# Performance work log

Measured on AMD Instinct MI355X. Metric: run time of the kernel, lower is better.

## Reference

```python
import jax, jax.numpy as jnp
import numpy as np

NUM_HEADS = 16


def setup_inputs() -> dict:
    key = jax.random.key(0)
    ks = jax.random.split(key, 7)
    T, B, E = 2048, 2, 1024
    return {
        "query": jax.random.normal(ks[0], (T, B, E), jnp.float32),
        "key": jax.random.normal(ks[1], (T, B, E), jnp.float32),
        "value": jax.random.normal(ks[2], (T, B, E), jnp.float32),
        "query_pos": jax.random.normal(ks[3], (T, B, E), jnp.float32),
        "key_pos": jax.random.normal(ks[4], (T, B, E), jnp.float32),
        "W": jax.random.normal(ks[5], (E, E), jnp.float32) * (1.0 / np.sqrt(E)),
        "b": jax.random.normal(ks[6], (E,), jnp.float32) * 0.01,
    }


def reference(query, key, value, query_pos, key_pos, W, b):
    T, B, E = query.shape
    S = key.shape[0]
    H = NUM_HEADS
    D = E // H
    scale = jnp.asarray(D ** 0.5, query.dtype)

    identity = query  # residual uses query BEFORE positional add
    q = query + query_pos
    k = key + key_pos

    # (T,B,E) -> (B,H,T,D)
    q = q.reshape(T, B, H, D).transpose(1, 2, 0, 3)
    k = k.reshape(S, B, H, D).transpose(1, 2, 0, 3)
    v = value.reshape(S, B, H, D).transpose(1, 2, 0, 3)

    attn = jnp.einsum("bhtd,bhsd->bhts", q, k) / scale
    attn = jax.nn.softmax(attn, axis=-1)  # dropout p=0 -> identity

    out = jnp.einsum("bhts,bhsd->bhtd", attn, v)
    out = out.transpose(2, 0, 1, 3).reshape(T, B, E)  # (B,H,T,D)->(T,B,E)
    out = out @ W.T + b  # fuse_heads linear; out_dropout p=0 -> identity
    out = out + identity

    attn_avg = attn.sum(axis=1) / H  # average over heads -> (B,T,S)
    return out, attn_avg
```

## Files before the change

### kernel.cpp

```cpp
#include <hip/hip_runtime.h>
#include <hip/hip_bf16.h>

#define T_DIM 2048
#define S_DIM 2048
#define B_DIM 2
#define E_DIM 1024
#define H_DIM 16
#define D_DIM 64
#define EXP2S 0.18033688f
#define EXP2(x) __builtin_amdgcn_exp2f(x)

typedef unsigned short u16;
typedef unsigned int u32;
typedef float v4f __attribute__((ext_vector_type(4)));
typedef short v8s __attribute__((ext_vector_type(8)));
typedef short v4s __attribute__((ext_vector_type(4)));

__device__ __forceinline__ u16 f2bf(float f) {
    union { float f; u32 u; } x; x.f = f;
    return (u16)((x.u + 0x7fffu + ((x.u >> 16) & 1u)) >> 16);
}
__device__ __forceinline__ u32 pkrn(float lo, float hi) {
    union { __hip_bfloat162 h; u32 u; } c;
    c.h = __float22bfloat162_rn(make_float2(lo, hi));
    return c.u;
}
__device__ __forceinline__ v4f mfma16(v8s a, v8s b, v4f c) {
    return __builtin_amdgcn_mfma_f32_16x16x32_bf16(a, b, c, 0, 0, 0);
}
__device__ __forceinline__ v4f mfma16x16(v4s a, v4s b, v4f c) {
    return __builtin_amdgcn_mfma_f32_16x16x16bf16_1k(a, b, c, 0, 0, 0);
}
__device__ __forceinline__ v8s ld8(const u16* p) {
    return *reinterpret_cast<const v8s*>(p);
}

__global__ __launch_bounds__(256) void prep_qk(
    const float* __restrict__ q, const float* __restrict__ qp,
    const float* __restrict__ k, const float* __restrict__ kp,
    const float* __restrict__ W,
    u16* __restrict__ qb, u16* __restrict__ ks, u16* __restrict__ Wb) {
    int o = blockIdx.x * 256 + threadIdx.x;
    int d = o & 63, t = (o >> 6) & 2047, h = (o >> 17) & 15, b = o >> 21;
    int src = ((t * B_DIM + b) << 10) + (h << 6) + d;
    qb[o] = f2bf((q[src] + qp[src]) * EXP2S);
    ks[o] = f2bf(k[src] + kp[src]);
    if (o < E_DIM * E_DIM) Wb[o] = f2bf(W[o]);
}

__global__ __launch_bounds__(256) void prep_vt(const float* __restrict__ V, u16* __restrict__ vt) {
    __shared__ float tile[64 * 65];
    int bx = blockIdx.x;
    int bh = bx >> 5;
    int s0 = (bx & 31) * 64;
    int b = bh >> 4, h = bh & 15;
    int tid = threadIdx.x;
    int quarter = tid >> 6, c = tid & 63;
    int boff = b * E_DIM + h * 64;
#pragma unroll
    for (int p = 0; p < 16; ++p) {
        int r = quarter * 16 + p;
        tile[r * 65 + c] = V[(size_t)(s0 + r) * (B_DIM * E_DIM) + boff + c];
    }
    __syncthreads();
#pragma unroll
    for (int p = 0; p < 16; ++p) {
        int d = quarter * 16 + p;
        vt[(size_t)bh * (D_DIM * S_DIM) + (size_t)d * S_DIM + s0 + c] = f2bf(tile[c * 65 + d]);
    }
}

#define PITCH 72
__global__ __launch_bounds__(256) void attn_pv(
    const u16* __restrict__ qb, const u16* __restrict__ ks, const u16* __restrict__ vt,
    float* __restrict__ lin, u16* __restrict__ Xb) {
    __shared__ u16 Kl[2][64 * PITCH];
    __shared__ u16 Vl[2][64 * PITCH];

    int bx = blockIdx.x;
    int bh = bx >> 4;
    int b = bh >> 4, h = bh & 15;
    int tid = threadIdx.x;
    int w = tid >> 6;
    int tbase = (bx & 15) * 128 + w * 32;
    int lane = tid & 63;
    int m = lane & 15, g = lane >> 4;

    int srow = tid >> 2;
    int sqtr = (tid & 3) * 16;

    uint4 kr0, kr1, vr0, vr1;
    auto load_stage = [&](int s0) {
        const uint4* kp = reinterpret_cast<const uint4*>(
            ks + ((size_t)bh * S_DIM + s0 + srow) * 64 + sqtr);
        kr0 = kp[0]; kr1 = kp[1];
        const uint4* vp = reinterpret_cast<const uint4*>(
            vt + (size_t)bh * (D_DIM * S_DIM) + (size_t)srow * S_DIM + s0 + sqtr);
        vr0 = vp[0]; vr1 = vp[1];
    };
    auto write_stage = [&](int buf) {
        uint4* kd = reinterpret_cast<uint4*>(&Kl[buf][srow * PITCH + sqtr]);
        kd[0] = kr0; kd[1] = kr1;
        uint4* vd = reinterpret_cast<uint4*>(&Vl[buf][srow * PITCH + sqtr]);
        vd[0] = vr0; vd[1] = vr1;
    };

    const u16* qrow = qb + ((size_t)bh * T_DIM + tbase + m) * 64 + g * 8;
    v8s aq[2][2];
    aq[0][0] = ld8(qrow);        aq[0][1] = ld8(qrow + 32);
    aq[1][0] = ld8(qrow + 1024); aq[1][1] = ld8(qrow + 1024 + 32);

    v4f O[2][4];
    float lacc[2] = {0.f, 0.f};
#pragma unroll
    for (int tr = 0; tr < 2; ++tr)
#pragma unroll
        for (int dd = 0; dd < 4; ++dd) O[tr][dd] = (v4f){0.f, 0.f, 0.f, 0.f};

    load_stage(0);
    write_stage(0);
    load_stage(64);
    __syncthreads();

    for (int it = 0; it < 32; ++it) {
        int buf = it & 1;
        const u16* Kb = Kl[buf];
        const u16* Vb = Vl[buf];
#pragma unroll
        for (int ss = 0; ss < 4; ++ss) {
            v8s kf0 = ld8(&Kb[(ss * 16 + m) * PITCH + g * 8]);
            v8s kf1 = ld8(&Kb[(ss * 16 + m) * PITCH + 32 + g * 8]);
            v4s pa0, pa1;
            {
                v4f z = {0.f, 0.f, 0.f, 0.f};
                z = mfma16(kf0, aq[0][0], z);
                z = mfma16(kf1, aq[0][1], z);
                float e0 = EXP2(z[0]);
                float e1 = EXP2(z[1]);
                float e2 = EXP2(z[2]);
                float e3 = EXP2(z[3]);
                lacc[0] += (e0 + e1) + (e2 + e3);
                union { u32 u[2]; v4s s; } pk_;
                pk_.u[0] = pkrn(e0, e1);
                pk_.u[1] = pkrn(e2, e3);
                pa0 = pk_.s;
            }
            {
                v4f z = {0.f, 0.f, 0.f, 0.f};
                z = mfma16(kf0, aq[1][0], z);
                z = mfma16(kf1, aq[1][1], z);
                float e0 = EXP2(z[0]);
                float e1 = EXP2(z[1]);
                float e2 = EXP2(z[2]);
                float e3 = EXP2(z[3]);
                lacc[1] += (e0 + e1) + (e2 + e3);
                union { u32 u[2]; v4s s; } pk_;
                pk_.u[0] = pkrn(e0, e1);
                pk_.u[1] = pkrn(e2, e3);
                pa1 = pk_.s;
            }
            __builtin_amdgcn_s_setprio(1);
#pragma unroll
            for (int dd = 0; dd < 4; ++dd) {
                v4s bv = *reinterpret_cast<const v4s*>(
                    &Vb[(dd * 16 + m) * PITCH + ss * 16 + g * 4]);
                O[0][dd] = mfma16x16(pa0, bv, O[0][dd]);
                O[1][dd] = mfma16x16(pa1, bv, O[1][dd]);
            }
            __builtin_amdgcn_s_setprio(0);
        }
        if (it + 1 < 32) {
            write_stage(buf ^ 1);
            if (it + 2 < 32) load_stage((it + 2) * 64);
        }
        __syncthreads();
    }

#pragma unroll
    for (int tr = 0; tr < 2; ++tr) {
        lacc[tr] += __shfl_xor(lacc[tr], 16);
        lacc[tr] += __shfl_xor(lacc[tr], 32);
        float linv = 1.0f / lacc[tr];
        if (lane < 16) lin[(size_t)bh * T_DIM + tbase + tr * 16 + m] = linv;
#pragma unroll
        for (int r = 0; r < 4; ++r) {
            float lr = __shfl(linv, g * 4 + r);
            int t = tbase + tr * 16 + g * 4 + r;
#pragma unroll
            for (int dd = 0; dd < 4; ++dd)
                Xb[((size_t)t * B_DIM + b) * E_DIM + h * 64 + dd * 16 + m] =
                    f2bf(O[tr][dd][r] * lr);
        }
    }
}

__global__ __launch_bounds__(256, 4) void attn_avg(
    const u16* __restrict__ qb, const u16* __restrict__ ks,
    const float* __restrict__ lin, float* __restrict__ out1) {
    __shared__ u16 Kl[2][64 * PITCH];
    int bx = blockIdx.x;
    int b = bx >> 9;
    int tt = (bx >> 5) & 15;
    int st = bx & 31;
    int tid = threadIdx.x;
    int w = tid >> 6;
    int tbase = tt * 128 + w * 32;
    int sbase = st * 64;
    int lane = tid & 63, m = lane & 15, g = lane >> 4;

    int srow = tid >> 2;
    int sqtr = (tid & 3) * 16;

    uint4 kr0, kr1;
    auto load_stage = [&](int h) {
        const uint4* kp = reinterpret_cast<const uint4*>(
            ks + ((size_t)(b * 16 + h) * S_DIM + sbase + srow) * 64 + sqtr);
        kr0 = kp[0]; kr1 = kp[1];
    };
    auto write_stage = [&](int buf) {
        uint4* kd = reinterpret_cast<uint4*>(&Kl[buf][srow * PITCH + sqtr]);
        kd[0] = kr0; kd[1] = kr1;
    };

    v8s aqc00, aqc01, aqc10, aqc11, aqn00, aqn01, aqn10, aqn11;
    float livc[2][4], livn[2][4];
    auto load_q = [&](int h, v8s& a00, v8s& a01, v8s& a10, v8s& a11, float (&liv)[2][4]) {
        int bh = b * 16 + h;
        const u16* qrow = qb + ((size_t)bh * T_DIM + tbase + m) * 64 + g * 8;
        a00 = ld8(qrow);        a01 = ld8(qrow + 32);
        a10 = ld8(qrow + 1024); a11 = ld8(qrow + 1024 + 32);
#pragma unroll
        for (int tr = 0; tr < 2; ++tr)
#pragma unroll
            for (int r = 0; r < 4; ++r)
                liv[tr][r] = lin[(size_t)bh * T_DIM + tbase + tr * 16 + g * 4 + r] * (1.0f / 16.0f);
    };

    v4f AVG[2][4];
#pragma unroll
    for (int tr = 0; tr < 2; ++tr)
#pragma unroll
        for (int ss = 0; ss < 4; ++ss) AVG[tr][ss] = (v4f){0.f, 0.f, 0.f, 0.f};

    load_stage(0);
    write_stage(0);
    load_stage(1);
    load_q(0, aqc00, aqc01, aqc10, aqc11, livc);
    __syncthreads();

    for (int h = 0; h < H_DIM; ++h) {
        int buf = h & 1;
        if (h + 1 < H_DIM) load_q(h + 1, aqn00, aqn01, aqn10, aqn11, livn);

        const u16* Kb = Kl[buf];
#pragma unroll
        for (int ss = 0; ss < 4; ++ss) {
            v8s kf0 = ld8(&Kb[(ss * 16 + m) * PITCH + g * 8]);
            v8s kf1 = ld8(&Kb[(ss * 16 + m) * PITCH + 32 + g * 8]);
            {
                v4f z = {0.f, 0.f, 0.f, 0.f};
                z = mfma16(aqc00, kf0, z);
                z = mfma16(aqc01, kf1, z);
#pragma unroll
                for (int r = 0; r < 4; ++r)
                    AVG[0][ss][r] += EXP2(z[r]) * livc[0][r];
            }
            {
                v4f z = {0.f, 0.f, 0.f, 0.f};
                z = mfma16(aqc10, kf0, z);
                z = mfma16(aqc11, kf1, z);
#pragma unroll
                for (int r = 0; r < 4; ++r)
                    AVG[1][ss][r] += EXP2(z[r]) * livc[1][r];
            }
        }
        if (h + 1 < H_DIM) {
            write_stage(buf ^ 1);
            if (h + 2 < H_DIM) load_stage(h + 2);
        }
        __syncthreads();
        aqc00 = aqn00; aqc01 = aqn01; aqc10 = aqn10; aqc11 = aqn11;
#pragma unroll
        for (int tr = 0; tr < 2; ++tr)
#pragma unroll
            for (int r = 0; r < 4; ++r) livc[tr][r] = livn[tr][r];
    }
#pragma unroll
    for (int tr = 0; tr < 2; ++tr)
#pragma unroll
        for (int ss = 0; ss < 4; ++ss)
#pragma unroll
            for (int r = 0; r < 4; ++r) {
                int t = tbase + tr * 16 + g * 4 + r;
                out1[((size_t)b * T_DIM + t) * S_DIM + sbase + ss * 16 + m] = AVG[tr][ss][r];
            }
}

__global__ __launch_bounds__(256) void linear_mfma(
    const u16* __restrict__ Xb, const u16* __restrict__ Wb,
    const float* __restrict__ bias, const float* __restrict__ query,
    float* __restrict__ out0) {
    __shared__ u16 Al[2][64 * PITCH];
    __shared__ u16 Wl[2][128 * PITCH];
    int bx = blockIdx.x;
    int it = bx >> 3, jt = bx & 7;
    int tid = threadIdx.x;
    int w = tid >> 6;
    int lane = tid & 63;
    int m = lane & 15, g = lane >> 4;

    int arow = tid >> 2, aq4 = (tid & 3) * 16;
    int wrow = tid >> 1, wh2 = (tid & 1) * 32;

    uint4 ar0, ar1, wr0, wr1, wr2, wr3;
    auto load_stage = [&](int k0) {
        const uint4* ap = reinterpret_cast<const uint4*>(
            Xb + (size_t)(it * 64 + arow) * E_DIM + k0 + aq4);
        ar0 = ap[0]; ar1 = ap[1];
        const uint4* wp = reinterpret_cast<const uint4*>(
            Wb + (size_t)(jt * 128 + wrow) * E_DIM + k0 + wh2);
        wr0 = wp[0]; wr1 = wp[1]; wr2 = wp[2]; wr3 = wp[3];
    };
    auto write_stage = [&](int buf) {
        uint4* ad = reinterpret_cast<uint4*>(&Al[buf][arow * PITCH + aq4]);
        ad[0] = ar0; ad[1] = ar1;
        uint4* wd = reinterpret_cast<uint4*>(&Wl[buf][wrow * PITCH + wh2]);
        wd[0] = wr0; wd[1] = wr1; wd[2] = wr2; wd[3] = wr3;
    };

    v4f acc[4][2];
#pragma unroll
    for (int tr = 0; tr < 4; ++tr)
#pragma unroll
        for (int nn = 0; nn < 2; ++nn) acc[tr][nn] = (v4f){0.f, 0.f, 0.f, 0.f};

    load_stage(0);
    write_stage(0);
    load_stage(64);
    __syncthreads();

    for (int itk = 0; itk < 16; ++itk) {
        int buf = itk & 1;
        const u16* Ab = Al[buf];
        const u16* Ws = Wl[buf];
        v8s af[4][2], wf[2][2];
#pragma unroll
        for (int tr = 0; tr < 4; ++tr) {
            af[tr][0] = ld8(&Ab[(tr * 16 + m) * PITCH + g * 8]);
            af[tr][1] = ld8(&Ab[(tr * 16 + m) * PITCH + 32 + g * 8]);
        }
#pragma unroll
        for (int nn = 0; nn < 2; ++nn) {
            wf[nn][0] = ld8(&Ws[((w * 2 + nn) * 16 + m) * PITCH + g * 8]);
            wf[nn][1] = ld8(&Ws[((w * 2 + nn) * 16 + m) * PITCH + 32 + g * 8]);
        }
#pragma unroll
        for (int tr = 0; tr < 4; ++tr)
#pragma unroll
            for (int nn = 0; nn < 2; ++nn) {
                acc[tr][nn] = mfma16(af[tr][0], wf[nn][0], acc[tr][nn]);
                acc[tr][nn] = mfma16(af[tr][1], wf[nn][1], acc[tr][nn]);
            }
        if (itk + 1 < 16) {
            write_stage(buf ^ 1);
            if (itk + 2 < 16) load_stage((itk + 2) * 64);
        }
        __syncthreads();
    }

#pragma unroll
    for (int tr = 0; tr < 4; ++tr)
#pragma unroll
        for (int nn = 0; nn < 2; ++nn) {
            int col = jt * 128 + (w * 2 + nn) * 16 + m;
            float bv = bias[col];
#pragma unroll
            for (int r = 0; r < 4; ++r) {
                int row = it * 64 + tr * 16 + g * 4 + r;
                out0[(size_t)row * E_DIM + col] =
                    acc[tr][nn][r] + bv + query[(size_t)row * E_DIM + col];
            }
        }
}

extern "C" void kernel_launch(void* const* d_in, const int* in_sizes, int n_in,
                              void* d_out, int out_size, void* d_ws, size_t ws_size,
                              hipStream_t stream) {
    const float* query = (const float*)d_in[0];
    const float* key   = (const float*)d_in[1];
    const float* value = (const float*)d_in[2];
    const float* qpos  = (const float*)d_in[3];
    const float* kpos  = (const float*)d_in[4];
    const float* W     = (const float*)d_in[5];
    const float* bias  = (const float*)d_in[6];

    char* ws = (char*)d_ws;
    u16*   qb  = (u16*)(ws);
    u16*   ks  = (u16*)(ws + (size_t)( 8u << 20));
    u16*   vt  = (u16*)(ws + (size_t)(16u << 20));
    u16*   Wb  = (u16*)(ws + (size_t)(24u << 20));
    float* lin = (float*)(ws + (size_t)(26u << 20));
    u16*   Xb  = (u16*)(ws + (size_t)(27u << 20));

    float* out0 = (float*)d_out;
    float* out1 = out0 + (size_t)T_DIM * B_DIM * E_DIM;

    prep_qk<<<(B_DIM * H_DIM * T_DIM * D_DIM) / 256, 256, 0, stream>>>(query, qpos, key, kpos, W, qb, ks, Wb);
    prep_vt<<<B_DIM * H_DIM * (S_DIM / 64), 256, 0, stream>>>(value, vt);
    attn_pv<<<B_DIM * H_DIM * (T_DIM / 128), 256, 0, stream>>>(qb, ks, vt, lin, Xb);
    attn_avg<<<B_DIM * (T_DIM / 128) * (S_DIM / 64), 256, 0, stream>>>(qb, ks, lin, out1);
    linear_mfma<<<(T_DIM * B_DIM / 64) * (E_DIM / 128), 256, 0, stream>>>(Xb, Wb, bias, query, out0);
}
```

Baseline: 258.8 us.

## Merge prep kernels and co-schedule attention-average with output linear in one launch

Combines the Q/K/W conversion and V transpose into a single launch with a block-index split. Likewise merges the head-averaged attention kernel with the output projection GEMM so their blocks can run concurrently, since neither depends on the other. The linear part now uses a 32-wide K step with a smaller LDS pitch so it fits the shared-memory budget of the avg part. It also drops the s_setprio hints in attn_pv. This trades launch overhead and tail idle time for more loop iterations and barriers in the GEMM.

```diff
diff --git a/kernel.cpp b/kernel.cpp
--- a/kernel.cpp
+++ b/kernel.cpp
@@ -35,26 +35,28 @@
     return *reinterpret_cast<const v8s*>(p);
 }
 
-__global__ __launch_bounds__(256) void prep_qk(
+__global__ __launch_bounds__(256) void prep_all(
     const float* __restrict__ q, const float* __restrict__ qp,
     const float* __restrict__ k, const float* __restrict__ kp,
-    const float* __restrict__ W,
-    u16* __restrict__ qb, u16* __restrict__ ks, u16* __restrict__ Wb) {
-    int o = blockIdx.x * 256 + threadIdx.x;
-    int d = o & 63, t = (o >> 6) & 2047, h = (o >> 17) & 15, b = o >> 21;
-    int src = ((t * B_DIM + b) << 10) + (h << 6) + d;
-    qb[o] = f2bf((q[src] + qp[src]) * EXP2S);
-    ks[o] = f2bf(k[src] + kp[src]);
-    if (o < E_DIM * E_DIM) Wb[o] = f2bf(W[o]);
-}
-
-__global__ __launch_bounds__(256) void prep_vt(const float* __restrict__ V, u16* __restrict__ vt) {
+    const float* __restrict__ W, const float* __restrict__ V,
+    u16* __restrict__ qb, u16* __restrict__ ks, u16* __restrict__ Wb,
+    u16* __restrict__ vt) {
     __shared__ float tile[64 * 65];
     int bx = blockIdx.x;
-    int bh = bx >> 5;
-    int s0 = (bx & 31) * 64;
+    int tid = threadIdx.x;
+    if (bx < 16384) {
+        int o = bx * 256 + tid;
+        int d = o & 63, t = (o >> 6) & 2047, h = (o >> 17) & 15, b = o >> 21;
+        int src = ((t * B_DIM + b) << 10) + (h << 6) + d;
+        qb[o] = f2bf((q[src] + qp[src]) * EXP2S);
+        ks[o] = f2bf(k[src] + kp[src]);
+        if (o < E_DIM * E_DIM) Wb[o] = f2bf(W[o]);
+        return;
+    }
+    int vb = bx - 16384;
+    int bh = vb >> 5;
+    int s0 = (vb & 31) * 64;
     int b = bh >> 4, h = bh & 15;
-    int tid = threadIdx.x;
     int quarter = tid >> 6, c = tid & 63;
     int boff = b * E_DIM + h * 64;
 #pragma unroll
@@ -159,7 +161,6 @@
                 pk_.u[1] = pkrn(e2, e3);
                 pa1 = pk_.s;
             }
-            __builtin_amdgcn_s_setprio(1);
 #pragma unroll
             for (int dd = 0; dd < 4; ++dd) {
                 v4s bv = *reinterpret_cast<const v4s*>(
@@ -167,7 +168,6 @@
                 O[0][dd] = mfma16x16(pa0, bv, O[0][dd]);
                 O[1][dd] = mfma16x16(pa1, bv, O[1][dd]);
             }
-            __builtin_amdgcn_s_setprio(0);
         }
         if (it + 1 < 32) {
             write_stage(buf ^ 1);
@@ -194,138 +194,136 @@
     }
 }
 
-__global__ __launch_bounds__(256, 4) void attn_avg(
+#define PITCHL 40
+__global__ __launch_bounds__(256, 4) void avg_linear(
     const u16* __restrict__ qb, const u16* __restrict__ ks,
-    const float* __restrict__ lin, float* __restrict__ out1) {
-    __shared__ u16 Kl[2][64 * PITCH];
-    int bx = blockIdx.x;
-    int b = bx >> 9;
-    int tt = (bx >> 5) & 15;
-    int st = bx & 31;
-    int tid = threadIdx.x;
-    int w = tid >> 6;
-    int tbase = tt * 128 + w * 32;
-    int sbase = st * 64;
-    int lane = tid & 63, m = lane & 15, g = lane >> 4;
-
-    int srow = tid >> 2;
-    int sqtr = (tid & 3) * 16;
-
-    uint4 kr0, kr1;
-    auto load_stage = [&](int h) {
-        const uint4* kp = reinterpret_cast<const uint4*>(
-            ks + ((size_t)(b * 16 + h) * S_DIM + sbase + srow) * 64 + sqtr);
-        kr0 = kp[0]; kr1 = kp[1];
-    };
-    auto write_stage = [&](int buf) {
-        uint4* kd = reinterpret_cast<uint4*>(&Kl[buf][srow * PITCH + sqtr]);
-        kd[0] = kr0; kd[1] = kr1;
-    };
-
-    v8s aqc00, aqc01, aqc10, aqc11, aqn00, aqn01, aqn10, aqn11;
-    float livc[2][4], livn[2][4];
-    auto load_q = [&](int h, v8s& a00, v8s& a01, v8s& a10, v8s& a11, float (&liv)[2][4]) {
-        int bh = b * 16 + h;
-        const u16* qrow = qb + ((size_t)bh * T_DIM + tbase + m) * 64 + g * 8;
-        a00 = ld8(qrow);        a01 = ld8(qrow + 32);
-        a10 = ld8(qrow + 1024); a11 = ld8(qrow + 1024 + 32);
-#pragma unroll
-        for (int tr = 0; tr < 2; ++tr)
-#pragma unroll
-            for (int r = 0; r < 4; ++r)
-                liv[tr][r] = lin[(size_t)bh * T_DIM + tbase + tr * 16 + g * 4 + r] * (1.0f / 16.0f);
-    };
-
-    v4f AVG[2][4];
-#pragma unroll
-    for (int tr = 0; tr < 2; ++tr)
-#pragma unroll
-        for (int ss = 0; ss < 4; ++ss) AVG[tr][ss] = (v4f){0.f, 0.f, 0.f, 0.f};
-
-    load_stage(0);
-    write_stage(0);
-    load_stage(1);
-    load_q(0, aqc00, aqc01, aqc10, aqc11, livc);
-    __syncthreads();
-
-    for (int h = 0; h < H_DIM; ++h) {
-        int buf = h & 1;
-        if (h + 1 < H_DIM) load_q(h + 1, aqn00, aqn01, aqn10, aqn11, livn);
-
-        const u16* Kb = Kl[buf];
-#pragma unroll
-        for (int ss = 0; ss < 4; ++ss) {
-            v8s kf0 = ld8(&Kb[(ss * 16 + m) * PITCH + g * 8]);
-            v8s kf1 = ld8(&Kb[(ss * 16 + m) * PITCH + 32 + g * 8]);
-            {
-                v4f z = {0.f, 0.f, 0.f, 0.f};
-                z = mfma16(aqc00, kf0, z);
-                z = mfma16(aqc01, kf1, z);
-#pragma unroll
-                for (int r = 0; r < 4; ++r)
-                    AVG[0][ss][r] += EXP2(z[r]) * livc[0][r];
-            }
-            {
-                v4f z = {0.f, 0.f, 0.f, 0.f};
-                z = mfma16(aqc10, kf0, z);
-                z = mfma16(aqc11, kf1, z);
-#pragma unroll
-                for (int r = 0; r < 4; ++r)
-                    AVG[1][ss][r] += EXP2(z[r]) * livc[1][r];
-            }
-        }
-        if (h + 1 < H_DIM) {
-            write_stage(buf ^ 1);
-            if (h + 2 < H_DIM) load_stage(h + 2);
-        }
-        __syncthreads();
-        aqc00 = aqn00; aqc01 = aqn01; aqc10 = aqn10; aqc11 = aqn11;
-#pragma unroll
-        for (int tr = 0; tr < 2; ++tr)
-#pragma unroll
-            for (int r = 0; r < 4; ++r) livc[tr][r] = livn[tr][r];
-    }
-#pragma unroll
-    for (int tr = 0; tr < 2; ++tr)
-#pragma unroll
-        for (int ss = 0; ss < 4; ++ss)
-#pragma unroll
-            for (int r = 0; r < 4; ++r) {
-                int t = tbase + tr * 16 + g * 4 + r;
-                out1[((size_t)b * T_DIM + t) * S_DIM + sbase + ss * 16 + m] = AVG[tr][ss][r];
-            }
-}
-
-__global__ __launch_bounds__(256) void linear_mfma(
+    const float* __restrict__ lin, float* __restrict__ out1,
     const u16* __restrict__ Xb, const u16* __restrict__ Wb,
     const float* __restrict__ bias, const float* __restrict__ query,
     float* __restrict__ out0) {
-    __shared__ u16 Al[2][64 * PITCH];
-    __shared__ u16 Wl[2][128 * PITCH];
+    __shared__ __align__(16) char smem[30720];
     int bx = blockIdx.x;
-    int it = bx >> 3, jt = bx & 7;
     int tid = threadIdx.x;
     int w = tid >> 6;
-    int lane = tid & 63;
-    int m = lane & 15, g = lane >> 4;
-
-    int arow = tid >> 2, aq4 = (tid & 3) * 16;
-    int wrow = tid >> 1, wh2 = (tid & 1) * 32;
-
-    uint4 ar0, ar1, wr0, wr1, wr2, wr3;
+    int lane = tid & 63, m = lane & 15, g = lane >> 4;
+
+    if (bx < 1024) {
+        u16* Kl0 = reinterpret_cast<u16*>(smem);
+        int b = bx >> 9;
+        int tt = (bx >> 5) & 15;
+        int st = bx & 31;
+        int tbase = tt * 128 + w * 32;
+        int sbase = st * 64;
+
+        int srow = tid >> 2;
+        int sqtr = (tid & 3) * 16;
+
+        uint4 kr0, kr1;
+        auto load_stage = [&](int h) {
+            const uint4* kp = reinterpret_cast<const uint4*>(
+                ks + ((size_t)(b * 16 + h) * S_DIM + sbase + srow) * 64 + sqtr);
+            kr0 = kp[0]; kr1 = kp[1];
+        };
+        auto write_stage = [&](int buf) {
+            uint4* kd = reinterpret_cast<uint4*>(&Kl0[buf * (64 * PITCH) + srow * PITCH + sqtr]);
+            kd[0] = kr0; kd[1] = kr1;
+        };
+
+        v8s aqc00, aqc01, aqc10, aqc11, aqn00, aqn01, aqn10, aqn11;
+        float livc[2][4], livn[2][4];
+        auto load_q = [&](int h, v8s& a00, v8s& a01, v8s& a10, v8s& a11, float (&liv)[2][4]) {
+            int bh = b * 16 + h;
+            const u16* qrow = qb + ((size_t)bh * T_DIM + tbase + m) * 64 + g * 8;
+            a00 = ld8(qrow);        a01 = ld8(qrow + 32);
+            a10 = ld8(qrow + 1024); a11 = ld8(qrow + 1024 + 32);
+#pragma unroll
+            for (int tr = 0; tr < 2; ++tr)
+#pragma unroll
+                for (int r = 0; r < 4; ++r)
+                    liv[tr][r] = lin[(size_t)bh * T_DIM + tbase + tr * 16 + g * 4 + r] * (1.0f / 16.0f);
+        };
+
+        v4f AVG[2][4];
+#pragma unroll
+        for (int tr = 0; tr < 2; ++tr)
+#pragma unroll
+            for (int ss = 0; ss < 4; ++ss) AVG[tr][ss] = (v4f){0.f, 0.f, 0.f, 0.f};
+
+        load_stage(0);
+        write_stage(0);
+        load_stage(1);
+        load_q(0, aqc00, aqc01, aqc10, aqc11, livc);
+        __syncthreads();
+
+        for (int h = 0; h < H_DIM; ++h) {
+            int buf = h & 1;
+            if (h + 1 < H_DIM) load_q(h + 1, aqn00, aqn01, aqn10, aqn11, livn);
+
+            const u16* Kb = &Kl0[buf * (64 * PITCH)];
+#pragma unroll
+            for (int ss = 0; ss < 4; ++ss) {
+                v8s kf0 = ld8(&Kb[(ss * 16 + m) * PITCH + g * 8]);
+                v8s kf1 = ld8(&Kb[(ss * 16 + m) * PITCH + 32 + g * 8]);
+                {
+                    v4f z = {0.f, 0.f, 0.f, 0.f};
+                    z = mfma16(aqc00, kf0, z);
+                    z = mfma16(aqc01, kf1, z);
+#pragma unroll
+                    for (int r = 0; r < 4; ++r)
+                        AVG[0][ss][r] += EXP2(z[r]) * livc[0][r];
+                }
+                {
+                    v4f z = {0.f, 0.f, 0.f, 0.f};
+                    z = mfma16(aqc10, kf0, z);
+                    z = mfma16(aqc11, kf1, z);
+#pragma unroll
+                    for (int r = 0; r < 4; ++r)
+                        AVG[1][ss][r] += EXP2(z[r]) * livc[1][r];
+                }
+            }
+            if (h + 1 < H_DIM) {
+                write_stage(buf ^ 1);
+                if (h + 2 < H_DIM) load_stage(h + 2);
+            }
+            __syncthreads();
+            aqc00 = aqn00; aqc01 = aqn01; aqc10 = aqn10; aqc11 = aqn11;
+#pragma unroll
+            for (int tr = 0; tr < 2; ++tr)
+#pragma unroll
+                for (int r = 0; r < 4; ++r) livc[tr][r] = livn[tr][r];
+        }
+#pragma unroll
+        for (int tr = 0; tr < 2; ++tr)
+#pragma unroll
+            for (int ss = 0; ss < 4; ++ss)
+#pragma unroll
+                for (int r = 0; r < 4; ++r) {
+                    int t = tbase + tr * 16 + g * 4 + r;
+                    out1[((size_t)b * T_DIM + t) * S_DIM + sbase + ss * 16 + m] = AVG[tr][ss][r];
+                }
+        return;
+    }
+
+    u16* Al = reinterpret_cast<u16*>(smem);
+    u16* Wl = reinterpret_cast<u16*>(smem) + 2 * 64 * PITCHL;
+    int lb = bx - 1024;
+    int it = lb >> 3, jt = lb & 7;
+
+    int arow = tid >> 2, ac = (tid & 3) * 8;
+    int wrow = tid >> 1, wc = (tid & 1) * 16;
+
+    uint4 ar0, wr0, wr1;
     auto load_stage = [&](int k0) {
-        const uint4* ap = reinterpret_cast<const uint4*>(
-            Xb + (size_t)(it * 64 + arow) * E_DIM + k0 + aq4);
-        ar0 = ap[0]; ar1 = ap[1];
+        ar0 = *reinterpret_cast<const uint4*>(
+            Xb + (size_t)(it * 64 + arow) * E_DIM + k0 + ac);
         const uint4* wp = reinterpret_cast<const uint4*>(
-            Wb + (size_t)(jt * 128 + wrow) * E_DIM + k0 + wh2);
-        wr0 = wp[0]; wr1 = wp[1]; wr2 = wp[2]; wr3 = wp[3];
+            Wb + (size_t)(jt * 128 + wrow) * E_DIM + k0 + wc);
+        wr0 = wp[0]; wr1 = wp[1];
     };
     auto write_stage = [&](int buf) {
-        uint4* ad = reinterpret_cast<uint4*>(&Al[buf][arow * PITCH + aq4]);
-        ad[0] = ar0; ad[1] = ar1;
-        uint4* wd = reinterpret_cast<uint4*>(&Wl[buf][wrow * PITCH + wh2]);
-        wd[0] = wr0; wd[1] = wr1; wd[2] = wr2; wd[3] = wr3;
+        *reinterpret_cast<uint4*>(&Al[buf * (64 * PITCHL) + arow * PITCHL + ac]) = ar0;
+        uint4* wd = reinterpret_cast<uint4*>(&Wl[buf * (128 * PITCHL) + wrow * PITCHL + wc]);
+        wd[0] = wr0; wd[1] = wr1;
     };
 
     v4f acc[4][2];
@@ -336,34 +334,28 @@
 
     load_stage(0);
     write_stage(0);
-    load_stage(64);
+    load_stage(32);
     __syncthreads();
 
-    for (int itk = 0; itk < 16; ++itk) {
+    for (int itk = 0; itk < 32; ++itk) {
         int buf = itk & 1;
-        const u16* Ab = Al[buf];
-        const u16* Ws = Wl[buf];
-        v8s af[4][2], wf[2][2];
-#pragma unroll
-        for (int tr = 0; tr < 4; ++tr) {
-            af[tr][0] = ld8(&Ab[(tr * 16 + m) * PITCH + g * 8]);
-            af[tr][1] = ld8(&Ab[(tr * 16 + m) * PITCH + 32 + g * 8]);
-        }
-#pragma unroll
-        for (int nn = 0; nn < 2; ++nn) {
-            wf[nn][0] = ld8(&Ws[((w * 2 + nn) * 16 + m) * PITCH + g * 8]);
-            wf[nn][1] = ld8(&Ws[((w * 2 + nn) * 16 + m) * PITCH + 32 + g * 8]);
-        }
+        const u16* Ab = &Al[buf * (64 * PITCHL)];
+        const u16* Ws = &Wl[buf * (128 * PITCHL)];
+        v8s af[4], wf[2];
 #pragma unroll
         for (int tr = 0; tr < 4; ++tr)
-#pragma unroll
-            for (int nn = 0; nn < 2; ++nn) {
-                acc[tr][nn] = mfma16(af[tr][0], wf[nn][0], acc[tr][nn]);
-                acc[tr][nn] = mfma16(af[tr][1], wf[nn][1], acc[tr][nn]);
-            }
-        if (itk + 1 < 16) {
+            af[tr] = ld8(&Ab[(tr * 16 + m) * PITCHL + g * 8]);
+#pragma unroll
+        for (int nn = 0; nn < 2; ++nn)
+            wf[nn] = ld8(&Ws[((w * 2 + nn) * 16 + m) * PITCHL + g * 8]);
+#pragma unroll
+        for (int tr = 0; tr < 4; ++tr)
+#pragma unroll
+            for (int nn = 0; nn < 2; ++nn)
+                acc[tr][nn] = mfma16(af[tr], wf[nn], acc[tr][nn]);
+        if (itk + 1 < 32) {
             write_stage(buf ^ 1);
-            if (itk + 2 < 16) load_stage((itk + 2) * 64);
+            if (itk + 2 < 32) load_stage((itk + 2) * 32);
         }
         __syncthreads();
     }
@@ -405,9 +397,9 @@
     float* out0 = (float*)d_out;
     float* out1 = out0 + (size_t)T_DIM * B_DIM * E_DIM;
 
-    prep_qk<<<(B_DIM * H_DIM * T_DIM * D_DIM) / 256, 256, 0, stream>>>(query, qpos, key, kpos, W, qb, ks, Wb);
-    prep_vt<<<B_DIM * H_DIM * (S_DIM / 64), 256, 0, stream>>>(value, vt);
+    prep_all<<<16384 + B_DIM * H_DIM * (S_DIM / 64), 256, 0, stream>>>(
+        query, qpos, key, kpos, W, value, qb, ks, Wb, vt);
     attn_pv<<<B_DIM * H_DIM * (T_DIM / 128), 256, 0, stream>>>(qb, ks, vt, lin, Xb);
-    attn_avg<<<B_DIM * (T_DIM / 128) * (S_DIM / 64), 256, 0, stream>>>(qb, ks, lin, out1);
-    linear_mfma<<<(T_DIM * B_DIM / 64) * (E_DIM / 128), 256, 0, stream>>>(Xb, Wb, bias, query, out0);
-}
+    avg_linear<<<B_DIM * (T_DIM / 128) * (S_DIM / 64) + (T_DIM * B_DIM / 64) * (E_DIM / 128),
+                 256, 0, stream>>>(qb, ks, lin, out1, Xb, Wb, bias, query, out0);
+}
```

Result: slower. 274.4 us (+6.0%).
